# Kernel optimization log

Measured on AMD Instinct MI355X. Metric: run time of the kernel, lower is better.

The kernel has to match this reference:

```python
import jax, jax.numpy as jnp
import numpy as np

LATENT_DIMENSION = 128
HIDDEN = 1024            # HIDDEN_SIZE + LATENT_DIMENSION
SONG_PIECE_SIZE = 128
SONG_LENGTH = 32768
T_STEPS = SONG_LENGTH // SONG_PIECE_SIZE  # 256
BATCH = 128


def setup_inputs() -> dict:
    key = jax.random.key(0)
    ks = jax.random.split(key, 7)
    s_ih = 1.0 / np.sqrt(HIDDEN)
    return {
        "current_batch_size": BATCH,
        "z": jax.random.normal(ks[0], (BATCH, 1, LATENT_DIMENSION), dtype=jnp.float32),
        "w_ih": jax.random.normal(ks[1], (4 * HIDDEN, LATENT_DIMENSION), dtype=jnp.float32) * s_ih,
        "w_hh": jax.random.normal(ks[2], (4 * HIDDEN, HIDDEN), dtype=jnp.float32) * s_ih,
        "b_ih": jax.random.normal(ks[3], (4 * HIDDEN,), dtype=jnp.float32) * s_ih,
        "b_hh": jax.random.normal(ks[4], (4 * HIDDEN,), dtype=jnp.float32) * s_ih,
        "W_fc": jax.random.normal(ks[5], (SONG_PIECE_SIZE, HIDDEN), dtype=jnp.float32) * s_ih,
        "b_fc": jax.random.normal(ks[6], (SONG_PIECE_SIZE,), dtype=jnp.float32) * s_ih,
    }


def _run(z, w_ih, w_hh, b_ih, b_hh, W_fc, b_fc):
    B = z.shape[0]
    # inputs per step: step 0 is z[:,0,:], remaining steps are zeros
    xs = jnp.concatenate(
        [z[:, 0:1, :].transpose(1, 0, 2),
         jnp.zeros((T_STEPS - 1, B, LATENT_DIMENSION), dtype=z.dtype)], axis=0)  # [T,B,L]
    h0 = jnp.zeros((B, HIDDEN), dtype=z.dtype)
    c0 = jnp.zeros((B, HIDDEN), dtype=z.dtype)

    def cell(carry, x):
        h, c = carry
        gates = x @ w_ih.T + b_ih + h @ w_hh.T + b_hh  # [B, 4H]
        i, f, g, o = jnp.split(gates, 4, axis=-1)       # PyTorch gate order i,f,g,o
        c_new = jax.nn.sigmoid(f) * c + jax.nn.sigmoid(i) * jnp.tanh(g)
        h_new = jax.nn.sigmoid(o) * jnp.tanh(c_new)
        y = h_new @ W_fc.T + b_fc                       # [B, SONG_PIECE_SIZE]
        return (h_new, c_new), y

    _, ys = jax.lax.scan(cell, (h0, c0), xs)            # ys: [T, B, P]
    return ys.transpose(1, 0, 2).reshape(B, SONG_LENGTH)


def reference(current_batch_size, z, w_ih, w_hh, b_ih, b_hh, W_fc, b_fc):
    return _run(z, w_ih, w_hh, b_ih, b_hh, W_fc, b_fc)
```

## Files before the change

### kernel.cpp

```cpp
#include <hip/hip_runtime.h>
#include <stdint.h>

#define BB   128
#define LL   128
#define HH   1024
#define G4   4096
#define TT   256
#define PP   128

#define NSL  64
#define NB   256
#define CARSL 56

typedef _Float16 half8  __attribute__((ext_vector_type(8)));
typedef float   floatx4 __attribute__((ext_vector_type(4)));

__device__ __forceinline__ float sigf(float x) {
  x = fminf(fmaxf(x, -30.f), 30.f);
  return 1.f / (1.f + __expf(-x));
}
__device__ __forceinline__ float tanhf_fast(float x) {
  x = fminf(fmaxf(x, -15.f), 15.f);
  float e = __expf(2.f * x);
  return (e - 1.f) / (e + 1.f);
}
__device__ __forceinline__ unsigned short f2h(float x) {
  _Float16 h = (_Float16)x;
  return __builtin_bit_cast(unsigned short, h);
}
__device__ __forceinline__ void store_h(unsigned short* p, float x) {
  __hip_atomic_store(p, f2h(x), __ATOMIC_RELAXED, __HIP_MEMORY_SCOPE_AGENT);
}

#define ALOAD(dst, base, IMM)                                              \
  asm volatile("global_load_dwordx4 %0, %1, off offset:%2 sc0 sc1"         \
               : "=&v"(dst) : "v"(base), "n"(IMM) : "memory")

#define KSTEP(kc, WN)                                                      \
  {                                                                        \
    asm volatile("s_waitcnt vmcnt(%2)"                                     \
                 : "+v"(ap0[(kc) & 15]), "+v"(ap1[(kc) & 15]) : "n"(WN));  \
    half8 a0 = ap0[(kc) & 15], a1 = ap1[(kc) & 15];                        \
    const int sw = ((kc) * 4 + quad) ^ rsw;                                \
    _Pragma("unroll")                                                      \
    for (int nt = 0; nt < NT; ++nt) {                                      \
      half8 b = (nt < NGATE) ? w8[(nt * 16 + l15) * 128 + sw] : fcb[kc];   \
      acc[0][nt] = __builtin_amdgcn_mfma_f32_16x16x32_f16(a0, b, acc[0][nt], 0, 0, 0); \
      acc[1][nt] = __builtin_amdgcn_mfma_f32_16x16x32_f16(a1, b, acc[1][nt], 0, 0, 0); \
    }                                                                      \
    if ((kc) < 16) {                                                       \
      ALOAD(ap0[(kc) & 15], p0, ((kc) + 16) * 64);                         \
      ALOAD(ap1[(kc) & 15], p1, ((kc) + 16) * 64);                         \
    }                                                                      \
  }

__device__ __forceinline__ void publish(unsigned* qf, int sl, unsigned v, int lane) {
  asm volatile("s_waitcnt vmcnt(0)" ::: "memory");
  if (lane == 0)
    __hip_atomic_store(qf + sl, v, __ATOMIC_RELAXED, __HIP_MEMORY_SCOPE_AGENT);
}
__device__ __forceinline__ void waitq(const unsigned* qf, unsigned tgt, int lane) {
  for (;;) {
    unsigned v = __hip_atomic_load(qf + lane, __ATOMIC_RELAXED, __HIP_MEMORY_SCOPE_AGENT);
    if (__all(v >= tgt)) break;
    __builtin_amdgcn_s_sleep(1);
  }
}

__global__ void prep_gates0(const float* __restrict__ z, const float* __restrict__ w_ih,
                            const float* __restrict__ b_ih, const float* __restrict__ b_hh,
                            float* __restrict__ g0) {
  int j = blockIdx.x;
  int b = threadIdx.x;
  const float* zr = z + b * LL;
  const float* wr = w_ih + (size_t)j * LL;
  float s = 0.f;
#pragma unroll 4
  for (int k = 0; k < LL; ++k) s += zr[k] * wr[k];
  g0[(size_t)b * G4 + j] = s + b_ih[j] + b_hh[j];
}

__global__ void prep_weights(const float* __restrict__ w_hh,
                             unsigned short* __restrict__ wbuf) {
  int R = blockIdx.x;
  int sl = R >> 6, rr = R & 63, tile = rr >> 4, nl = rr & 15;
  int g = (tile == 0) ? 0 : (tile == 1) ? 2 : (tile == 2) ? 1 : 3;
  const float* src = w_hh + (size_t)(g * HH + sl * 16 + nl) * HH;
  int rsw = nl & 7;
  unsigned short* dst = wbuf + (size_t)R * HH;
  for (int k = threadIdx.x; k < HH; k += blockDim.x) {
    int dk = (((k >> 3) ^ rsw) << 3) | (k & 7);
    _Float16 v = (_Float16)src[k];
    dst[dk] = __builtin_bit_cast(unsigned short, v);
  }
}

template <int NT, int NGATE>
__device__ __forceinline__ void gemmK(const unsigned short* __restrict__ hb,
                                      const half8* __restrict__ w8,
                                      const half8 (&fcb)[32],
                                      int au0, int au1,
                                      int quad, int rsw, int l15,
                                      floatx4 acc[2][NT]) {
  const unsigned short* p0 = hb + au0;
  const unsigned short* p1 = hb + au1;
  half8 ap0[16], ap1[16];
  ALOAD(ap0[0],  p0, 0);    ALOAD(ap1[0],  p1, 0);
  ALOAD(ap0[1],  p0, 64);   ALOAD(ap1[1],  p1, 64);
  ALOAD(ap0[2],  p0, 128);  ALOAD(ap1[2],  p1, 128);
  ALOAD(ap0[3],  p0, 192);  ALOAD(ap1[3],  p1, 192);
  ALOAD(ap0[4],  p0, 256);  ALOAD(ap1[4],  p1, 256);
  ALOAD(ap0[5],  p0, 320);  ALOAD(ap1[5],  p1, 320);
  ALOAD(ap0[6],  p0, 384);  ALOAD(ap1[6],  p1, 384);
  ALOAD(ap0[7],  p0, 448);  ALOAD(ap1[7],  p1, 448);
  ALOAD(ap0[8],  p0, 512);  ALOAD(ap1[8],  p1, 512);
  ALOAD(ap0[9],  p0, 576);  ALOAD(ap1[9],  p1, 576);
  ALOAD(ap0[10], p0, 640);  ALOAD(ap1[10], p1, 640);
  ALOAD(ap0[11], p0, 704);  ALOAD(ap1[11], p1, 704);
  ALOAD(ap0[12], p0, 768);  ALOAD(ap1[12], p1, 768);
  ALOAD(ap0[13], p0, 832);  ALOAD(ap1[13], p1, 832);
  ALOAD(ap0[14], p0, 896);  ALOAD(ap1[14], p1, 896);
  ALOAD(ap0[15], p0, 960);  ALOAD(ap1[15], p1, 960);
  KSTEP(0, 30)  KSTEP(1, 30)  KSTEP(2, 30)  KSTEP(3, 30)
  KSTEP(4, 30)  KSTEP(5, 30)  KSTEP(6, 30)  KSTEP(7, 30)
  KSTEP(8, 30)  KSTEP(9, 30)  KSTEP(10, 30) KSTEP(11, 30)
  KSTEP(12, 30) KSTEP(13, 30) KSTEP(14, 30) KSTEP(15, 30)
  KSTEP(16, 30) KSTEP(17, 28) KSTEP(18, 26) KSTEP(19, 24)
  KSTEP(20, 22) KSTEP(21, 20) KSTEP(22, 18) KSTEP(23, 16)
  KSTEP(24, 14) KSTEP(25, 12) KSTEP(26, 10) KSTEP(27, 8)
  KSTEP(28, 6)  KSTEP(29, 4)  KSTEP(30, 2)  KSTEP(31, 0)
}

__global__ __launch_bounds__(64, 1) void lstm_persist(
    const float* __restrict__ g0,
    const unsigned short* __restrict__ wbuf,
    const float* __restrict__ b_ih, const float* __restrict__ b_hh,
    const float* __restrict__ W_fc, const float* __restrict__ b_fc,
    float* __restrict__ out,
    unsigned short* __restrict__ hbuf,
    unsigned* __restrict__ ctl) {
  extern __shared__ __align__(16) unsigned short sW[];
  const int tid  = threadIdx.x;
  const int lane = tid;
  const int quad = lane >> 4;
  const int l15  = lane & 15;
  const int bid  = blockIdx.x;
  const int sl   = bid >> 2;
  const int q    = bid & 3;
  const int mbase = q * 32;
  const int rsw  = l15 & 7;
  const bool carrier = (sl >= CARSL);
  const int pcol = (sl - CARSL) * 16 + l15;

  unsigned* qf = ctl + q * 1024;

  {
    const uint4* s4 = (const uint4*)(wbuf + (size_t)sl * 64 * HH);
    uint4* d4 = (uint4*)sW;
    for (int i = tid; i < 64 * HH / 8; i += 64) d4[i] = s4[i];
  }
  __syncthreads();
  const half8* w8 = (const half8*)sW;
  const floatx4 z4 = {0.f, 0.f, 0.f, 0.f};

  half8 fcb[32];
  float biasf = 0.f;
  if (carrier) {
    biasf = b_fc[pcol];
    const float* wp = W_fc + (size_t)pcol * HH + quad * 8;
#pragma unroll
    for (int kc = 0; kc < 32; ++kc) {
      float4 f0 = *(const float4*)(wp + kc * 32);
      float4 f1 = *(const float4*)(wp + kc * 32 + 4);
      half8 hv;
      hv[0] = (_Float16)f0.x; hv[1] = (_Float16)f0.y;
      hv[2] = (_Float16)f0.z; hv[3] = (_Float16)f0.w;
      hv[4] = (_Float16)f1.x; hv[5] = (_Float16)f1.y;
      hv[6] = (_Float16)f1.z; hv[7] = (_Float16)f1.w;
      fcb[kc] = hv;
    }
  }

  const int u = sl * 16 + l15;
  const float bi = b_ih[u]          + b_hh[u];
  const float bf = b_ih[HH + u]     + b_hh[HH + u];
  const float bg = b_ih[2*HH + u]   + b_hh[2*HH + u];
  const float bo = b_ih[3*HH + u]   + b_hh[3*HH + u];
  float c[2][4] = {{0,0,0,0},{0,0,0,0}};

#pragma unroll
  for (int mt = 0; mt < 2; ++mt)
#pragma unroll
    for (int r = 0; r < 4; ++r) {
      const int m = mbase + mt * 16 + quad * 4 + r;
      const float* gr = g0 + (size_t)m * G4;
      float iv = gr[u], gv = gr[2 * HH + u], ov = gr[3 * HH + u];
      float ct = sigf(iv) * tanhf_fast(gv);
      c[mt][r] = ct;
      store_h(hbuf + (size_t)m * HH + u, sigf(ov) * tanhf_fast(ct));
    }
  publish(qf, sl, 1u, lane);

  const int au0 = (mbase +      l15) * HH + quad * 8;
  const int au1 = (mbase + 16 + l15) * HH + quad * 8;

  if (carrier) {
    for (int t = 1; t < TT; ++t) {
      waitq(qf, (unsigned)t, lane);
      const unsigned short* hb = hbuf + (size_t)((t - 1) & 1) * BB * HH;
      unsigned short* hw = hbuf + (size_t)(t & 1) * BB * HH;
      floatx4 acc[2][5] = {{z4, z4, z4, z4, z4}, {z4, z4, z4, z4, z4}};
      gemmK<5, 4>(hb, w8, fcb, au0, au1, quad, rsw, l15, acc);
#pragma unroll
      for (int mt = 0; mt < 2; ++mt)
#pragma unroll
        for (int r = 0; r < 4; ++r) {
          float iv = sigf(acc[mt][0][r] + bi);
          float gv = tanhf_fast(acc[mt][1][r] + bg);
          float fv = sigf(acc[mt][2][r] + bf);
          float ov = sigf(acc[mt][3][r] + bo);
          float ct = fv * c[mt][r] + iv * gv;
          c[mt][r] = ct;
          const int m = mbase + mt * 16 + quad * 4 + r;
          store_h(hw + (size_t)m * HH + u, ov * tanhf_fast(ct));
          out[(size_t)m * (TT * PP) + (size_t)(t - 1) * PP + pcol] =
              acc[mt][4][r] + biasf;
        }
      publish(qf, sl, (unsigned)(t + 1), lane);
    }
    waitq(qf, (unsigned)TT, lane);
    {
      const unsigned short* hb = hbuf + (size_t)((TT - 1) & 1) * BB * HH;
      floatx4 acc[2][1] = {{z4}, {z4}};
      gemmK<1, 0>(hb, w8, fcb, au0, au1, quad, rsw, l15, acc);
#pragma unroll
      for (int mt = 0; mt < 2; ++mt)
#pragma unroll
        for (int r = 0; r < 4; ++r) {
          const int m = mbase + mt * 16 + quad * 4 + r;
          out[(size_t)m * (TT * PP) + (size_t)(TT - 1) * PP + pcol] =
              acc[mt][0][r] + biasf;
        }
    }
  } else {
    for (int t = 1; t < TT; ++t) {
      waitq(qf, (unsigned)t, lane);
      const unsigned short* hb = hbuf + (size_t)((t - 1) & 1) * BB * HH;
      unsigned short* hw = hbuf + (size_t)(t & 1) * BB * HH;
      floatx4 acc[2][4] = {{z4, z4, z4, z4}, {z4, z4, z4, z4}};
      gemmK<4, 4>(hb, w8, fcb, au0, au1, quad, rsw, l15, acc);
#pragma unroll
      for (int mt = 0; mt < 2; ++mt)
#pragma unroll
        for (int r = 0; r < 4; ++r) {
          float iv = sigf(acc[mt][0][r] + bi);
          float gv = tanhf_fast(acc[mt][1][r] + bg);
          float fv = sigf(acc[mt][2][r] + bf);
          float ov = sigf(acc[mt][3][r] + bo);
          float ct = fv * c[mt][r] + iv * gv;
          c[mt][r] = ct;
          const int m = mbase + mt * 16 + quad * 4 + r;
          store_h(hw + (size_t)m * HH + u, ov * tanhf_fast(ct));
        }
      publish(qf, sl, (unsigned)(t + 1), lane);
    }
  }
}

extern "C" void kernel_launch(void* const* d_in, const int* in_sizes, int n_in,
                              void* d_out, int out_size, void* d_ws, size_t ws_size,
                              hipStream_t stream) {
  const float* z    = (const float*)d_in[1];
  const float* w_ih = (const float*)d_in[2];
  const float* w_hh = (const float*)d_in[3];
  const float* b_ih = (const float*)d_in[4];
  const float* b_hh = (const float*)d_in[5];
  const float* W_fc = (const float*)d_in[6];
  const float* b_fc = (const float*)d_in[7];
  float* out = (float*)d_out;

  char* ws = (char*)d_ws;
  unsigned*       ctl  = (unsigned*)ws;
  unsigned short* hbuf = (unsigned short*)(ws + 65536);
  float*          g0   = (float*)(ws + 65536 + (size_t)2 * BB * HH * 2);
  unsigned short* wbuf = (unsigned short*)(ws + 65536 + (size_t)2 * BB * HH * 2
                                              + (size_t)BB * G4 * 4);

  (void)hipFuncSetAttribute(reinterpret_cast<const void*>(lstm_persist),
                            hipFuncAttributeMaxDynamicSharedMemorySize, 160 * 1024);

  hipMemsetAsync(ctl, 0, 65536, stream);
  prep_gates0 <<<dim3(G4), dim3(BB), 0, stream>>>(z, w_ih, b_ih, b_hh, g0);
  prep_weights<<<dim3(NSL * 64), dim3(256), 0, stream>>>(w_hh, wbuf);
  lstm_persist<<<dim3(NB), dim3(64), 128 * 1024, stream>>>(g0, wbuf, b_ih, b_hh,
                                                           W_fc, b_fc, out, hbuf, ctl);
}
```

Baseline: 2.349 ms.

## Use per-timestep h buffers so h loads can use cached (sc0-only) reads

When the workspace is large enough, the hidden-state buffer gets a separate slot for every timestep instead of a double buffer. Since a slot is never overwritten, the h loads drop the sc1 bit and can be served from cache rather than bypassing it. This targets the latency of the per-step h reads on the recurrent critical path. It costs a much larger workspace (about 64 MB for h), and correctness relies on stale cache lines never being hit for freshly written slots. It falls back to the old path if the workspace is too small.

```diff
diff --git a/kernel.cpp b/kernel.cpp
--- a/kernel.cpp
+++ b/kernel.cpp
@@ -12,6 +12,7 @@
 #define NB   256
 #define CARSL 56
 
+
 typedef _Float16 half8  __attribute__((ext_vector_type(8)));
 typedef float   floatx4 __attribute__((ext_vector_type(4)));
 
@@ -32,9 +33,15 @@
   __hip_atomic_store(p, f2h(x), __ATOMIC_RELAXED, __HIP_MEMORY_SCOPE_AGENT);
 }
 
-#define ALOAD(dst, base, IMM)                                              \
-  asm volatile("global_load_dwordx4 %0, %1, off offset:%2 sc0 sc1"         \
-               : "=&v"(dst) : "v"(base), "n"(IMM) : "memory")
+template <bool CACHED, int IMM>
+__device__ __forceinline__ void ld16(half8& dst, const unsigned short* base) {
+  if constexpr (CACHED)
+    asm volatile("global_load_dwordx4 %0, %1, off offset:%2 sc0"
+                 : "=&v"(dst) : "v"(base), "n"(IMM) : "memory");
+  else
+    asm volatile("global_load_dwordx4 %0, %1, off offset:%2 sc0 sc1"
+                 : "=&v"(dst) : "v"(base), "n"(IMM) : "memory");
+}
 
 #define KSTEP(kc, WN)                                                      \
   {                                                                        \
@@ -49,8 +56,8 @@
       acc[1][nt] = __builtin_amdgcn_mfma_f32_16x16x32_f16(a1, b, acc[1][nt], 0, 0, 0); \
     }                                                                      \
     if ((kc) < 16) {                                                       \
-      ALOAD(ap0[(kc) & 15], p0, ((kc) + 16) * 64);                         \
-      ALOAD(ap1[(kc) & 15], p1, ((kc) + 16) * 64);                         \
+      ld16<CACHED, ((kc) + 16) * 64>(ap0[(kc) & 15], p0);                  \
+      ld16<CACHED, ((kc) + 16) * 64>(ap1[(kc) & 15], p1);                  \
     }                                                                      \
   }
 
@@ -95,7 +102,7 @@
   }
 }
 
-template <int NT, int NGATE>
+template <bool CACHED, int NT, int NGATE>
 __device__ __forceinline__ void gemmK(const unsigned short* __restrict__ hb,
                                       const half8* __restrict__ w8,
                                       const half8 (&fcb)[32],
@@ -105,22 +112,22 @@
   const unsigned short* p0 = hb + au0;
   const unsigned short* p1 = hb + au1;
   half8 ap0[16], ap1[16];
-  ALOAD(ap0[0],  p0, 0);    ALOAD(ap1[0],  p1, 0);
-  ALOAD(ap0[1],  p0, 64);   ALOAD(ap1[1],  p1, 64);
-  ALOAD(ap0[2],  p0, 128);  ALOAD(ap1[2],  p1, 128);
-  ALOAD(ap0[3],  p0, 192);  ALOAD(ap1[3],  p1, 192);
-  ALOAD(ap0[4],  p0, 256);  ALOAD(ap1[4],  p1, 256);
-  ALOAD(ap0[5],  p0, 320);  ALOAD(ap1[5],  p1, 320);
-  ALOAD(ap0[6],  p0, 384);  ALOAD(ap1[6],  p1, 384);
-  ALOAD(ap0[7],  p0, 448);  ALOAD(ap1[7],  p1, 448);
-  ALOAD(ap0[8],  p0, 512);  ALOAD(ap1[8],  p1, 512);
-  ALOAD(ap0[9],  p0, 576);  ALOAD(ap1[9],  p1, 576);
-  ALOAD(ap0[10], p0, 640);  ALOAD(ap1[10], p1, 640);
-  ALOAD(ap0[11], p0, 704);  ALOAD(ap1[11], p1, 704);
-  ALOAD(ap0[12], p0, 768);  ALOAD(ap1[12], p1, 768);
-  ALOAD(ap0[13], p0, 832);  ALOAD(ap1[13], p1, 832);
-  ALOAD(ap0[14], p0, 896);  ALOAD(ap1[14], p1, 896);
-  ALOAD(ap0[15], p0, 960);  ALOAD(ap1[15], p1, 960);
+  ld16<CACHED, 0>(ap0[0], p0);     ld16<CACHED, 0>(ap1[0], p1);
+  ld16<CACHED, 64>(ap0[1], p0);    ld16<CACHED, 64>(ap1[1], p1);
+  ld16<CACHED, 128>(ap0[2], p0);   ld16<CACHED, 128>(ap1[2], p1);
+  ld16<CACHED, 192>(ap0[3], p0);   ld16<CACHED, 192>(ap1[3], p1);
+  ld16<CACHED, 256>(ap0[4], p0);   ld16<CACHED, 256>(ap1[4], p1);
+  ld16<CACHED, 320>(ap0[5], p0);   ld16<CACHED, 320>(ap1[5], p1);
+  ld16<CACHED, 384>(ap0[6], p0);   ld16<CACHED, 384>(ap1[6], p1);
+  ld16<CACHED, 448>(ap0[7], p0);   ld16<CACHED, 448>(ap1[7], p1);
+  ld16<CACHED, 512>(ap0[8], p0);   ld16<CACHED, 512>(ap1[8], p1);
+  ld16<CACHED, 576>(ap0[9], p0);   ld16<CACHED, 576>(ap1[9], p1);
+  ld16<CACHED, 640>(ap0[10], p0);  ld16<CACHED, 640>(ap1[10], p1);
+  ld16<CACHED, 704>(ap0[11], p0);  ld16<CACHED, 704>(ap1[11], p1);
+  ld16<CACHED, 768>(ap0[12], p0);  ld16<CACHED, 768>(ap1[12], p1);
+  ld16<CACHED, 832>(ap0[13], p0);  ld16<CACHED, 832>(ap1[13], p1);
+  ld16<CACHED, 896>(ap0[14], p0);  ld16<CACHED, 896>(ap1[14], p1);
+  ld16<CACHED, 960>(ap0[15], p0);  ld16<CACHED, 960>(ap1[15], p1);
   KSTEP(0, 30)  KSTEP(1, 30)  KSTEP(2, 30)  KSTEP(3, 30)
   KSTEP(4, 30)  KSTEP(5, 30)  KSTEP(6, 30)  KSTEP(7, 30)
   KSTEP(8, 30)  KSTEP(9, 30)  KSTEP(10, 30) KSTEP(11, 30)
@@ -131,6 +138,7 @@
   KSTEP(28, 6)  KSTEP(29, 4)  KSTEP(30, 2)  KSTEP(31, 0)
 }
 
+template <bool CACHED>
 __global__ __launch_bounds__(64, 1) void lstm_persist(
     const float* __restrict__ g0,
     const unsigned short* __restrict__ wbuf,
@@ -207,10 +215,11 @@
   if (carrier) {
     for (int t = 1; t < TT; ++t) {
       waitq(qf, (unsigned)t, lane);
-      const unsigned short* hb = hbuf + (size_t)((t - 1) & 1) * BB * HH;
-      unsigned short* hw = hbuf + (size_t)(t & 1) * BB * HH;
+      const unsigned short* hb = hbuf +
+          (size_t)(CACHED ? (t - 1) : ((t - 1) & 1)) * BB * HH;
+      unsigned short* hw = hbuf + (size_t)(CACHED ? t : (t & 1)) * BB * HH;
       floatx4 acc[2][5] = {{z4, z4, z4, z4, z4}, {z4, z4, z4, z4, z4}};
-      gemmK<5, 4>(hb, w8, fcb, au0, au1, quad, rsw, l15, acc);
+      gemmK<CACHED, 5, 4>(hb, w8, fcb, au0, au1, quad, rsw, l15, acc);
 #pragma unroll
       for (int mt = 0; mt < 2; ++mt)
 #pragma unroll
@@ -230,9 +239,10 @@
     }
     waitq(qf, (unsigned)TT, lane);
     {
-      const unsigned short* hb = hbuf + (size_t)((TT - 1) & 1) * BB * HH;
+      const unsigned short* hb = hbuf +
+          (size_t)(CACHED ? (TT - 1) : ((TT - 1) & 1)) * BB * HH;
       floatx4 acc[2][1] = {{z4}, {z4}};
-      gemmK<1, 0>(hb, w8, fcb, au0, au1, quad, rsw, l15, acc);
+      gemmK<CACHED, 1, 0>(hb, w8, fcb, au0, au1, quad, rsw, l15, acc);
 #pragma unroll
       for (int mt = 0; mt < 2; ++mt)
 #pragma unroll
@@ -245,10 +255,11 @@
   } else {
     for (int t = 1; t < TT; ++t) {
       waitq(qf, (unsigned)t, lane);
-      const unsigned short* hb = hbuf + (size_t)((t - 1) & 1) * BB * HH;
-      unsigned short* hw = hbuf + (size_t)(t & 1) * BB * HH;
+      const unsigned short* hb = hbuf +
+          (size_t)(CACHED ? (t - 1) : ((t - 1) & 1)) * BB * HH;
+      unsigned short* hw = hbuf + (size_t)(CACHED ? t : (t & 1)) * BB * HH;
       floatx4 acc[2][4] = {{z4, z4, z4, z4}, {z4, z4, z4, z4}};
-      gemmK<4, 4>(hb, w8, fcb, au0, au1, quad, rsw, l15, acc);
+      gemmK<CACHED, 4, 4>(hb, w8, fcb, au0, au1, quad, rsw, l15, acc);
 #pragma unroll
       for (int mt = 0; mt < 2; ++mt)
 #pragma unroll
@@ -279,19 +290,32 @@
   const float* b_fc = (const float*)d_in[7];
   float* out = (float*)d_out;
 
+  const size_t ctlB   = 65536;
+  const size_t hFull  = (size_t)TT * BB * HH * 2;
+  const size_t hMin   = (size_t)2  * BB * HH * 2;
+  const size_t g0B    = (size_t)BB * G4 * 4;
+  const size_t wbufB  = (size_t)NSL * 64 * HH * 2;
+  const bool cached = ws_size >= ctlB + hFull + g0B + wbufB;
+  const size_t hB = cached ? hFull : hMin;
+
   char* ws = (char*)d_ws;
   unsigned*       ctl  = (unsigned*)ws;
-  unsigned short* hbuf = (unsigned short*)(ws + 65536);
-  float*          g0   = (float*)(ws + 65536 + (size_t)2 * BB * HH * 2);
-  unsigned short* wbuf = (unsigned short*)(ws + 65536 + (size_t)2 * BB * HH * 2
-                                              + (size_t)BB * G4 * 4);
-
-  (void)hipFuncSetAttribute(reinterpret_cast<const void*>(lstm_persist),
+  unsigned short* hbuf = (unsigned short*)(ws + ctlB);
+  float*          g0   = (float*)(ws + ctlB + hB);
+  unsigned short* wbuf = (unsigned short*)(ws + ctlB + hB + g0B);
+
+  (void)hipFuncSetAttribute(reinterpret_cast<const void*>(lstm_persist<true>),
                             hipFuncAttributeMaxDynamicSharedMemorySize, 160 * 1024);
-
-  hipMemsetAsync(ctl, 0, 65536, stream);
+  (void)hipFuncSetAttribute(reinterpret_cast<const void*>(lstm_persist<false>),
+                            hipFuncAttributeMaxDynamicSharedMemorySize, 160 * 1024);
+
+  hipMemsetAsync(ctl, 0, ctlB, stream);
   prep_gates0 <<<dim3(G4), dim3(BB), 0, stream>>>(z, w_ih, b_ih, b_hh, g0);
   prep_weights<<<dim3(NSL * 64), dim3(256), 0, stream>>>(w_hh, wbuf);
-  lstm_persist<<<dim3(NB), dim3(64), 128 * 1024, stream>>>(g0, wbuf, b_ih, b_hh,
-                                                           W_fc, b_fc, out, hbuf, ctl);
-}
+  if (cached)
+    lstm_persist<true><<<dim3(NB), dim3(64), 128 * 1024, stream>>>(
+        g0, wbuf, b_ih, b_hh, W_fc, b_fc, out, hbuf, ctl);
+  else
+    lstm_persist<false><<<dim3(NB), dim3(64), 128 * 1024, stream>>>(
+        g0, wbuf, b_ih, b_hh, W_fc, b_fc, out, hbuf, ctl);
+}
```

Result: no change. 2.330 ms (-0.8%).
